# Optimization experiments

Measured on AMD Instinct MI355X. Metric: run time of the kernel, lower is better.

Reference implementation:

```python
import jax, jax.numpy as jnp
from jax import lax
import numpy as np

COST_CLASS, COST_BBOX, COST_GIOU = 2.0, 5.0, 2.0
ALPHA, GAMMA, OTA_K = 0.25, 2.0, 5
EXPANDED_STRIDES = 32.0
DEG = 180.0 / np.pi


def _make_corners(key, prefix):
    k1, k2, k3, k4, k5 = jax.random.split(key, 5)
    cx = jax.random.uniform(k1, prefix, minval=0.0, maxval=512.0)
    cy = jax.random.uniform(k2, prefix, minval=0.0, maxval=512.0)
    w = jax.random.uniform(k3, prefix, minval=8.0, maxval=128.0)
    h = jax.random.uniform(k4, prefix, minval=8.0, maxval=128.0)
    ang = jax.random.uniform(k5, prefix, minval=0.0, maxval=np.pi)
    offs = jnp.array([[-0.5, -0.5], [0.5, -0.5], [0.5, 0.5], [-0.5, 0.5]], jnp.float32)
    wh = jnp.stack([w, h], -1)[..., None, :]          # [..., 1, 2]
    pts = offs * wh                                    # [..., 4, 2]
    c, s = jnp.cos(ang)[..., None], jnp.sin(ang)[..., None]
    rx = pts[..., 0] * c - pts[..., 1] * s + cx[..., None]
    ry = pts[..., 0] * s + pts[..., 1] * c + cy[..., None]
    return jnp.stack([rx, ry], -1).reshape(prefix + (8,))


def setup_inputs() -> dict:
    key = jax.random.key(0)
    k1, k2, k3, k4 = jax.random.split(key, 4)
    B, Q, G, C = 16, 4096, 128, 80
    return {
        "pred_logits": jax.random.normal(k1, (B, Q, C), jnp.float32),
        "pred_boxes": _make_corners(k2, (B, Q)),
        "gt_boxes": _make_corners(k3, (B, G)),
        "gt_labels": jax.random.randint(k4, (B, G), 0, C),
    }


def corners_to_cxcywha(c):  # [N,8] -> [N,5]
    xc = (c[:, 0] + c[:, 2] + c[:, 4] + c[:, 6]) / 4
    yc = (c[:, 1] + c[:, 3] + c[:, 5] + c[:, 7]) / 4
    w = jnp.sqrt((c[:, 0] - c[:, 2]) ** 2 + (c[:, 1] - c[:, 3]) ** 2)
    h = jnp.sqrt((c[:, 2] - c[:, 4]) ** 2 + (c[:, 3] - c[:, 5]) ** 2)
    ang = jnp.arctan2(c[:, 3] - c[:, 1], c[:, 2] - c[:, 0]) * DEG
    return jnp.stack([xc, yc, w, h, ang], 1)


def _aabb(b5):
    cx, cy, w, h = b5[:, 0], b5[:, 1], b5[:, 2], b5[:, 3]
    return jnp.stack([cx - w / 2, cy - h / 2, cx + w / 2, cy + h / 2], 1)


def pairwise_iou(b1, b2):
    a, b = _aabb(b1), _aabb(b2)
    lt = jnp.maximum(a[:, None, :2], b[None, :, :2])
    rb = jnp.minimum(a[:, None, 2:], b[None, :, 2:])
    wh = jnp.clip(rb - lt, 0.0)
    inter = wh[..., 0] * wh[..., 1]
    area1 = (a[:, 2] - a[:, 0]) * (a[:, 3] - a[:, 1])
    area2 = (b[:, 2] - b[:, 0]) * (b[:, 3] - b[:, 1])
    return inter / (area1[:, None] + area2[None, :] - inter + 1e-8)


def pairwise_diou(b1, b2):
    iou = pairwise_iou(b1, b2)
    a, b = _aabb(b1), _aabb(b2)
    enc = jnp.maximum(a[:, None, 2:], b[None, :, 2:]) - jnp.minimum(a[:, None, :2], b[None, :, :2])
    c2 = (enc ** 2).sum(-1) + 1e-8
    d2 = ((b1[:, None, :2] - b2[None, :, :2]) ** 2).sum(-1)
    return iou - d2 / c2


def get_in_boxes_info(boxes, gts):
    bc = boxes.reshape(-1, 4, 2).mean(1)   # [Q,2]
    gp = gts.reshape(-1, 4, 2)             # [G,4,2]
    gc = gp.mean(1)                        # [G,2]
    cdist = jnp.sqrt(((bc[:, None] - gc[None]) ** 2).sum(-1))  # [Q,G]
    v1 = gp[:, 1] - gp[:, 0]
    v2 = gp[:, 2] - gp[:, 0]
    gt_area = jnp.abs(v1[:, 0] * v2[:, 1] - v1[:, 1] * v2[:, 0]) / 2
    diag = jnp.sqrt(((gp.max(1) - gp.min(1)) ** 2).sum(-1))
    radius = diag / EXPANDED_STRIDES
    in_boxes = cdist <= (gt_area / radius)[None, :]
    in_centers = cdist <= radius[None, :]
    return in_boxes.any(1), in_boxes & in_centers


def _dedup(cost, m):
    multi = m.sum(1) > 1
    onehot = jax.nn.one_hot(jnp.argmin(cost, 1), cost.shape[1], dtype=m.dtype)
    return jnp.where(multi[:, None], onehot, m)


def _match_single(logits, pboxes, gboxes, glabels):
    Q, G = pboxes.shape[0], gboxes.shape[0]
    prob = jax.nn.sigmoid(logits)
    fg_mask, _ = get_in_boxes_info(pboxes, gboxes)
    p5, g5 = corners_to_cxcywha(pboxes), corners_to_cxcywha(gboxes)
    ious = pairwise_iou(p5, g5)
    neg = (1 - ALPHA) * prob ** GAMMA * -jnp.log(1 - prob + 1e-8)
    pos = ALPHA * (1 - prob) ** GAMMA * -jnp.log(prob + 1e-8)
    cost_class = (pos - neg)[:, glabels]                         # [Q,G]
    cost_bbox = jnp.abs(pboxes[:, None] - gboxes[None]).sum(-1)  # L1 cdist on corners
    cost_giou = -pairwise_diou(p5, g5)
    # NB: source has `+ self.cost_giou * -cost_giou`, i.e. +w*diou; replicated verbatim.
    cost = COST_BBOX * cost_bbox + COST_CLASS * cost_class + COST_GIOU * (-cost_giou)
    cost = cost + 10000.0 * (~fg_mask)[:, None].astype(cost.dtype)
    # dynamic-k: sum of top OTA_K ious per gt, truncated to int, min 1
    topk = lax.top_k(ious.T, OTA_K)[0]                 # [G, k]
    dyn_k = jnp.clip(topk.sum(-1).astype(jnp.int32), 1, Q)
    ranks = jnp.argsort(jnp.argsort(cost, axis=0), axis=0)  # ascending-cost rank per column
    matching = (ranks < dyn_k[None, :]).astype(cost.dtype)
    matching = _dedup(cost, matching)
    # ensure every gt matched (bounded replication of the while loop)
    def cond(carry):
        c, m, it = carry
        return jnp.any(m.sum(0) == 0) & (it < G)
    def body(carry):
        c, m, it = carry
        c = c + 100000.0 * (m.sum(1) > 0)[:, None].astype(c.dtype)
        unm = m.sum(0) == 0
        amin = jnp.argmin(c, 0)                          # [G]
        hit = (jnp.arange(Q)[:, None] == amin[None, :]) & unm[None, :]
        m = jnp.where(hit, 1.0, m)
        m = _dedup(c, m)
        return (c, m, it + 1)
    _, matching, _ = lax.while_loop(cond, body, (cost, matching, jnp.int32(0)))
    return matching, cost, ious


def reference(pred_logits, pred_boxes, gt_boxes, gt_labels):
    return jax.vmap(_match_single)(pred_logits, pred_boxes, gt_boxes, gt_labels)
```

## Files before the change

kernel.cpp:

```cpp
#include <hip/hip_runtime.h>
#include <cstdint>
#include <cstddef>

#define B_ 16
#define Q_ 4096
#define G_ 128
#define C_ 80
#define QCHUNK 32
#define NCH (Q_ / QCHUNK)

typedef unsigned long long u64;
#define U64MAX 0xffffffffffffffffull

__device__ __forceinline__ u64 packkey(float v, int q) {
    unsigned int bts = __float_as_uint(v);
    if (bts == 0x80000000u) bts = 0u;
    bts = (bts & 0x80000000u) ? ~bts : (bts | 0x80000000u);
    return ((u64)bts << 32) | (unsigned int)q;
}

__device__ __forceinline__ u64 umin64(u64 a, u64 b) { return a < b ? a : b; }
__device__ __forceinline__ u64 umax64(u64 a, u64 b) { return a > b ? a : b; }

__device__ __forceinline__ void merge5_desc(
    float& a0, float& a1, float& a2, float& a3, float& a4,
    float b0, float b1, float b2, float b3, float b4)
{
    const float r0 = fmaxf(a0, b0);
    const float r1 = fmaxf(fmaxf(a1, b1), fminf(a0, b0));
    const float r2 = fmaxf(fmaxf(a2, b2), fmaxf(fminf(a0, b1), fminf(a1, b0)));
    const float r3 = fmaxf(fmaxf(a3, b3),
                     fmaxf(fminf(a0, b2), fmaxf(fminf(a1, b1), fminf(a2, b0))));
    const float r4 = fmaxf(fmaxf(a4, b4),
                     fmaxf(fmaxf(fminf(a0, b3), fminf(a3, b0)),
                           fmaxf(fminf(a1, b2), fminf(a2, b1))));
    a0 = r0; a1 = r1; a2 = r2; a3 = r3; a4 = r4;
}

__device__ __forceinline__ void merge5_asc(
    u64& a0, u64& a1, u64& a2, u64& a3, u64& a4,
    u64 b0, u64 b1, u64 b2, u64 b3, u64 b4)
{
    const u64 r0 = umin64(a0, b0);
    const u64 r1 = umin64(umin64(a1, b1), umax64(a0, b0));
    const u64 r2 = umin64(umin64(a2, b2), umin64(umax64(a0, b1), umax64(a1, b0)));
    const u64 r3 = umin64(umin64(a3, b3),
                   umin64(umax64(a0, b2), umin64(umax64(a1, b1), umax64(a2, b0))));
    const u64 r4 = umin64(umin64(a4, b4),
                   umin64(umin64(umax64(a0, b3), umax64(a3, b0)),
                          umin64(umax64(a1, b2), umax64(a2, b1))));
    a0 = r0; a1 = r1; a2 = r2; a3 = r3; a4 = r4;
}

__global__ __launch_bounds__(256) void posneg_kernel(
    const float* __restrict__ logits, float* __restrict__ posneg)
{
    const int i = blockIdx.x * 256 + threadIdx.x;
    const float x = logits[i];
    float p;
    if (x >= 0.f) { const float e = expf(-x); p = 1.f / (1.f + e); }
    else          { const float e = expf(x);  p = e / (1.f + e); }
    const float pos = 0.25f * (1.f - p) * (1.f - p) * (-logf(p + 1e-8f));
    const float neg = 0.75f * p * p * (-logf(1.f - p + 1e-8f));
    posneg[i] = pos - neg;
}

__global__ __launch_bounds__(256) void fused_cost_kernel(
    const float* __restrict__ posneg,
    const float* __restrict__ pboxes,
    const float* __restrict__ gboxes,
    const int*   __restrict__ glabels,
    float* __restrict__ out_cost,
    float* __restrict__ out_iou,
    float* __restrict__ costT,
    float* __restrict__ piou)
{
    const int tid = threadIdx.x;
    const int g   = tid & 127;
    const int qh  = tid >> 7;
    const int ci  = blockIdx.x, b = blockIdx.y;
    const int q0  = ci * QCHUNK;

    __shared__ float pq[QCHUNK][16];
    __shared__ int   fgf[QCHUNK];
    __shared__ float lbuf[16 * 80];
    __shared__ float ctile[QCHUNK][G_ + 1];
    __shared__ float phalf[G_][5];

    const float4* gb4 = (const float4*)(gboxes + ((size_t)b * G_ + g) * 8);
    const float4 gA = gb4[0], gB = gb4[1];
    const float g0 = gA.x, g1 = gA.y, g2 = gA.z, g3 = gA.w;
    const float g4 = gB.x, g5 = gB.y, g6 = gB.z, g7 = gB.w;
    const float gxc = (g0 + g2 + g4 + g6) * 0.25f;
    const float gyc = (g1 + g3 + g5 + g7) * 0.25f;
    const float gw = sqrtf((g0 - g2) * (g0 - g2) + (g1 - g3) * (g1 - g3));
    const float gh = sqrtf((g2 - g4) * (g2 - g4) + (g3 - g5) * (g3 - g5));
    const float gax0 = gxc - gw * 0.5f, gay0 = gyc - gh * 0.5f;
    const float gax1 = gxc + gw * 0.5f, gay1 = gyc + gh * 0.5f;
    const float garea = (gax1 - gax0) * (gay1 - gay0);
    const float v1x = g2 - g0, v1y = g3 - g1, v2x = g4 - g0, v2y = g5 - g1;
    const float gt_area = fabsf(v1x * v2y - v1y * v2x) * 0.5f;
    const float mxx = fmaxf(fmaxf(g0, g2), fmaxf(g4, g6));
    const float mnx = fminf(fminf(g0, g2), fminf(g4, g6));
    const float mxy = fmaxf(fmaxf(g1, g3), fmaxf(g5, g7));
    const float mny = fminf(fminf(g1, g3), fminf(g5, g7));
    const float dgx = mxx - mnx, dgy = mxy - mny;
    const float radius = sqrtf(dgx * dgx + dgy * dgy) / 32.0f;
    const float thresh = gt_area / radius;
    const int lab = glabels[b * G_ + g];

    if (tid < 64) {
        const float4 v = ((const float4*)(pboxes + ((size_t)b * Q_ + q0) * 8))[tid];
        *(float4*)&pq[tid >> 1][(tid & 1) * 4] = v;
    }
    __syncthreads();
    if (tid < QCHUNK) {
        const float* pr = pq[tid];
        const float p0 = pr[0], p1 = pr[1], p2 = pr[2], p3 = pr[3];
        const float p4 = pr[4], p5v = pr[5], p6 = pr[6], p7 = pr[7];
        const float pxc = (p0 + p2 + p4 + p6) * 0.25f;
        const float pyc = (p1 + p3 + p5v + p7) * 0.25f;
        const float pw = sqrtf((p0 - p2) * (p0 - p2) + (p1 - p3) * (p1 - p3));
        const float ph = sqrtf((p2 - p4) * (p2 - p4) + (p3 - p5v) * (p3 - p5v));
        pq[tid][8]  = pxc;
        pq[tid][9]  = pyc;
        pq[tid][10] = pxc - pw * 0.5f;
        pq[tid][11] = pyc - ph * 0.5f;
        pq[tid][12] = pxc + pw * 0.5f;
        pq[tid][13] = pyc + ph * 0.5f;
        pq[tid][14] = pw * ph;
        fgf[tid] = 0;
    }
    __syncthreads();

    const int lane0 = ((tid & 63) == 0);
    for (int i = 0; i < QCHUNK / 2; ++i) {
        const int ql = 2 * i + qh;
        const float dx = pq[ql][8] - gxc, dy = pq[ql][9] - gyc;
        const int in = sqrtf(dx * dx + dy * dy) <= thresh;
        const int anyin = __any(in);
        if (anyin && lane0) fgf[ql] = 1;
    }

    float t0 = -1e38f, t1 = -1e38f, t2 = -1e38f, t3 = -1e38f, t4 = -1e38f;

    for (int sc = 0; sc < QCHUNK / 16; ++sc) {
        __syncthreads();
        for (int j = tid; j < 16 * 80; j += 256)
            lbuf[j] = posneg[((size_t)b * Q_ + q0 + sc * 16) * 80 + j];
        __syncthreads();
        #pragma unroll
        for (int jj = 0; jj < 8; ++jj) {
            const int ql = sc * 16 + 2 * jj + qh;
            const int q  = q0 + ql;
            const float4 prA = *(const float4*)&pq[ql][0];
            const float4 prB = *(const float4*)&pq[ql][4];
            const float4 prC = *(const float4*)&pq[ql][8];
            const float4 prD = *(const float4*)&pq[ql][12];
            const float p0 = prA.x, p1 = prA.y, p2 = prA.z, p3 = prA.w;
            const float p4 = prB.x, p5v = prB.y, p6 = prB.z, p7 = prB.w;
            const float pxc = prC.x, pyc = prC.y;
            const float pax0 = prC.z, pay0 = prC.w, pax1 = prD.x, pay1 = prD.y;
            const float parea = prD.z;

            const float l1 = fabsf(p0 - g0) + fabsf(p1 - g1) + fabsf(p2 - g2)
                           + fabsf(p3 - g3) + fabsf(p4 - g4) + fabsf(p5v - g5)
                           + fabsf(p6 - g6) + fabsf(p7 - g7);

            const float ltx = fmaxf(pax0, gax0), lty = fmaxf(pay0, gay0);
            const float rbx = fminf(pax1, gax1), rby = fminf(pay1, gay1);
            const float iw = fmaxf(rbx - ltx, 0.f), ih = fmaxf(rby - lty, 0.f);
            const float inter = iw * ih;
            const float iou = inter / (parea + garea - inter + 1e-8f);

            const float ew = fmaxf(pax1, gax1) - fminf(pax0, gax0);
            const float eh = fmaxf(pay1, gay1) - fminf(pay0, gay0);
            const float cc2 = ew * ew + eh * eh + 1e-8f;
            const float dx = pxc - gxc, dy = pyc - gyc;
            const float diou = iou - (dx * dx + dy * dy) / cc2;

            const float cclass = lbuf[(2 * jj + qh) * 80 + lab];
            const float cost = 5.f * l1 + 2.f * cclass + 2.f * diou
                             + (fgf[ql] ? 0.f : 10000.f);

            const size_t o = ((size_t)b * Q_ + q) * G_ + g;
            out_cost[o] = cost;
            out_iou[o]  = iou;
            ctile[ql][g] = cost;

            if (iou > t4) {
                if (iou > t0)      { t4 = t3; t3 = t2; t2 = t1; t1 = t0; t0 = iou; }
                else if (iou > t1) { t4 = t3; t3 = t2; t2 = t1; t1 = iou; }
                else if (iou > t2) { t4 = t3; t3 = t2; t2 = iou; }
                else if (iou > t3) { t4 = t3; t3 = iou; }
                else               { t4 = iou; }
            }
        }
    }

    if (qh == 1) {
        phalf[g][0] = t0; phalf[g][1] = t1; phalf[g][2] = t2;
        phalf[g][3] = t3; phalf[g][4] = t4;
    }
    __syncthreads();
    if (qh == 0) {
        merge5_desc(t0, t1, t2, t3, t4,
                    phalf[g][0], phalf[g][1], phalf[g][2], phalf[g][3], phalf[g][4]);
        const size_t pbase = (((size_t)b * G_ + g) * NCH + ci) * 5;
        piou[pbase + 0] = t0; piou[pbase + 1] = t1; piou[pbase + 2] = t2;
        piou[pbase + 3] = t3; piou[pbase + 4] = t4;
    }

    for (int t = tid; t < QCHUNK * G_ / 4; t += 256) {
        const int gg = t >> 3;
        const int k  = (t & 7) << 2;
        float4 o;
        o.x = ctile[k + 0][gg]; o.y = ctile[k + 1][gg];
        o.z = ctile[k + 2][gg]; o.w = ctile[k + 3][gg];
        *(float4*)&costT[((size_t)b * G_ + gg) * Q_ + q0 + k] = o;
    }
}

__global__ __launch_bounds__(256) void ramin_kernel(
    const float* __restrict__ cost, int* __restrict__ ramin)
{
    const int wv = threadIdx.x >> 6, ln = threadIdx.x & 63;
    const int row = blockIdx.x * 4 + wv;
    const float2 c2v = ((const float2*)(cost + (size_t)row * G_))[ln];
    float v; int gg;
    if (c2v.x <= c2v.y) { v = c2v.x; gg = 2 * ln; }
    else                { v = c2v.y; gg = 2 * ln + 1; }
    for (int off = 32; off > 0; off >>= 1) {
        const float ov = __shfl_xor(v, off);
        const int   og = __shfl_xor(gg, off);
        if (ov < v || (ov == v && og < gg)) { v = ov; gg = og; }
    }
    if (ln == 0) ramin[row] = gg;
}

__global__ __launch_bounds__(256) void dynk_scatter_kernel(
    const float* __restrict__ costT,
    const float* __restrict__ piou,
    u64* __restrict__ cand,
    int* __restrict__ cnt,
    int* __restrict__ gsel)
{
    const int col = blockIdx.x;
    const int b = col >> 7, g = col & 127;
    const int tid = threadIdx.x;
    const int wv = tid >> 6, ln = tid & 63;

    __shared__ u64 wl[4][5];

    const float4* colp = (const float4*)(costT + (size_t)col * Q_);
    u64 k0 = U64MAX, k1 = U64MAX, k2 = U64MAX, k3 = U64MAX, k4 = U64MAX;
    #pragma unroll
    for (int s = 0; s < 4; ++s) {
        const int idx = tid + s * 256;
        const float4 c4 = colp[idx];
        const int qb = idx * 4;
        const float vv[4] = {c4.x, c4.y, c4.z, c4.w};
        #pragma unroll
        for (int j = 0; j < 4; ++j) {
            const u64 kk = packkey(vv[j], qb + j);
            if (kk < k4) {
                if (kk < k0)      { k4 = k3; k3 = k2; k2 = k1; k1 = k0; k0 = kk; }
                else if (kk < k1) { k4 = k3; k3 = k2; k2 = k1; k1 = kk; }
                else if (kk < k2) { k4 = k3; k3 = k2; k2 = kk; }
                else if (kk < k3) { k4 = k3; k3 = kk; }
                else              { k4 = kk; }
            }
        }
    }
    #pragma unroll
    for (int off = 1; off < 64; off <<= 1) {
        merge5_asc(k0, k1, k2, k3, k4,
                   __shfl_xor(k0, off), __shfl_xor(k1, off), __shfl_xor(k2, off),
                   __shfl_xor(k3, off), __shfl_xor(k4, off));
    }
    if (ln == 0) { wl[wv][0] = k0; wl[wv][1] = k1; wl[wv][2] = k2; wl[wv][3] = k3; wl[wv][4] = k4; }
    __syncthreads();

    float t0 = -1e38f, t1 = -1e38f, t2 = -1e38f, t3 = -1e38f, t4 = -1e38f;
    if (tid < 64) {
        const size_t base = (size_t)col * (NCH * 5) + (size_t)tid * 10;
        t0 = piou[base + 0]; t1 = piou[base + 1]; t2 = piou[base + 2];
        t3 = piou[base + 3]; t4 = piou[base + 4];
        merge5_desc(t0, t1, t2, t3, t4,
                    piou[base + 5], piou[base + 6], piou[base + 7],
                    piou[base + 8], piou[base + 9]);
        #pragma unroll
        for (int off = 1; off < 64; off <<= 1) {
            merge5_desc(t0, t1, t2, t3, t4,
                        __shfl_xor(t0, off), __shfl_xor(t1, off), __shfl_xor(t2, off),
                        __shfl_xor(t3, off), __shfl_xor(t4, off));
        }
    }

    if (tid == 0) {
        u64 f0 = wl[0][0], f1 = wl[0][1], f2 = wl[0][2], f3 = wl[0][3], f4 = wl[0][4];
        merge5_asc(f0, f1, f2, f3, f4, wl[1][0], wl[1][1], wl[1][2], wl[1][3], wl[1][4]);
        merge5_asc(f0, f1, f2, f3, f4, wl[2][0], wl[2][1], wl[2][2], wl[2][3], wl[2][4]);
        merge5_asc(f0, f1, f2, f3, f4, wl[3][0], wl[3][1], wl[3][2], wl[3][3], wl[3][4]);
        cand[(size_t)col * 5 + 0] = f0;
        cand[(size_t)col * 5 + 1] = f1;
        cand[(size_t)col * 5 + 2] = f2;
        cand[(size_t)col * 5 + 3] = f3;
        cand[(size_t)col * 5 + 4] = f4;

        const float s = t0 + t1 + t2 + t3 + t4;
        int dynk = (int)s;
        if (dynk < 1) dynk = 1;
        if (dynk > 5) dynk = 5;
        const u64 ks[5] = {f0, f1, f2, f3, f4};
        #pragma unroll
        for (int i = 0; i < 5; ++i) {
            if (i < dynk) {
                const int q = (int)(ks[i] & 0xffffffffu);
                atomicAdd(&cnt[b * Q_ + q], 1);
                gsel[b * Q_ + q] = g;
            }
        }
    }
}

__global__ __launch_bounds__(256) void loop_kernel(
    const float* __restrict__ costT,
    const int* __restrict__ cnt,
    const int* __restrict__ gsel,
    const int* __restrict__ ramin,
    const u64* __restrict__ cand,
    int* __restrict__ rmatch_final)
{
    const int b = blockIdx.x, tid = threadIdx.x;
    const int wv = tid >> 6, ln = tid & 63;

    __shared__ short rmatch[Q_];
    __shared__ unsigned char s_ra[Q_];
    __shared__ int newh[Q_];
    __shared__ unsigned char newg[Q_];
    __shared__ u64 scand[G_][5];
    __shared__ int ptrs[G_], col_cnt[G_], unm_list[G_], prop[G_], fb_slot[G_], touched[G_];
    __shared__ int n_unm, n_fb, n_touch;

    for (int q = tid; q < Q_; q += 256) {
        const int c  = cnt[b * Q_ + q];
        const int ra = ramin[b * Q_ + q];
        s_ra[q] = (unsigned char)ra;
        newh[q] = 0;
        rmatch[q] = (c == 0) ? (short)-1
                             : (c == 1 ? (short)gsel[b * Q_ + q] : (short)ra);
    }
    if (tid < G_) { col_cnt[tid] = 0; ptrs[tid] = 0; }
    for (int i = tid; i < G_ * 5; i += 256)
        scand[i / 5][i % 5] = cand[(size_t)b * G_ * 5 + i];
    __syncthreads();
    for (int q = tid; q < Q_; q += 256)
        if (rmatch[q] >= 0) atomicAdd(&col_cnt[rmatch[q]], 1);
    __syncthreads();

    for (int it = 0; it < G_; ++it) {
        if (tid == 0) { n_unm = 0; n_fb = 0; n_touch = 0; }
        __syncthreads();
        if (tid < G_ && col_cnt[tid] == 0)
            unm_list[atomicAdd(&n_unm, 1)] = tid;
        __syncthreads();
        const int nu = n_unm;
        if (nu == 0) break;

        if (tid < nu) {
            const int g = unm_list[tid];
            int p = ptrs[g];
            int q = -1;
            while (p < 5) {
                const int cq = (int)(scand[g][p] & 0xffffffffu);
                if (rmatch[cq] < 0) { q = cq; break; }
                ++p;
            }
            ptrs[g] = p;
            prop[tid] = q;
            if (q < 0) fb_slot[atomicAdd(&n_fb, 1)] = tid;
        }
        __syncthreads();

        const int nf = n_fb;
        for (int i = wv; i < nf; i += 4) {
            const int slot = fb_slot[i];
            const int g = unm_list[slot];
            const float4* colp = (const float4*)(costT + ((size_t)b * G_ + g) * Q_);
            u64 k0 = U64MAX, k1 = U64MAX, k2 = U64MAX, k3 = U64MAX, k4 = U64MAX;
            #pragma unroll 4
            for (int s = 0; s < Q_ / 256; ++s) {
                const int idx = ln + s * 64;
                const float4 c4 = colp[idx];
                const int qb = idx * 4;
                const float vv[4] = {c4.x, c4.y, c4.z, c4.w};
                #pragma unroll
                for (int j = 0; j < 4; ++j) {
                    if (rmatch[qb + j] < 0) {
                        const u64 kk = packkey(vv[j], qb + j);
                        if (kk < k4) {
                            if (kk < k0)      { k4 = k3; k3 = k2; k2 = k1; k1 = k0; k0 = kk; }
                            else if (kk < k1) { k4 = k3; k3 = k2; k2 = k1; k1 = kk; }
                            else if (kk < k2) { k4 = k3; k3 = k2; k2 = kk; }
                            else if (kk < k3) { k4 = k3; k3 = kk; }
                            else              { k4 = kk; }
                        }
                    }
                }
            }
            #pragma unroll
            for (int off = 1; off < 64; off <<= 1) {
                merge5_asc(k0, k1, k2, k3, k4,
                           __shfl_xor(k0, off), __shfl_xor(k1, off), __shfl_xor(k2, off),
                           __shfl_xor(k3, off), __shfl_xor(k4, off));
            }
            if (ln == 0) {
                scand[g][0] = k0; scand[g][1] = k1; scand[g][2] = k2;
                scand[g][3] = k3; scand[g][4] = k4;
                ptrs[g] = 0;
                prop[slot] = (int)(k0 & 0xffffffffu);
            }
        }
        __syncthreads();

        if (tid < nu) {
            const int q = prop[tid];
            newg[q] = (unsigned char)unm_list[tid];
            if (atomicAdd(&newh[q], 1) == 0)
                touched[atomicAdd(&n_touch, 1)] = q;
        }
        __syncthreads();

        const int nt = n_touch;
        if (tid < nt) {
            const int q = touched[tid];
            const int nh = newh[q];
            const int gg = (nh == 1) ? (int)newg[q] : (int)s_ra[q];
            rmatch[q] = (short)gg;
            atomicAdd(&col_cnt[gg], 1);
            newh[q] = 0;
        }
        __syncthreads();
    }

    for (int q = tid; q < Q_; q += 256)
        rmatch_final[b * Q_ + q] = rmatch[q];
}

__global__ __launch_bounds__(256) void expand_kernel(
    const int* __restrict__ rmatch_final, float* __restrict__ out_match)
{
    const int idx = blockIdx.x * 256 + threadIdx.x;
    const int row = idx >> 5;
    const int gb  = (idx & 31) << 2;
    const int rm  = rmatch_final[row];
    float4 o;
    o.x = (rm == gb)     ? 1.f : 0.f;
    o.y = (rm == gb + 1) ? 1.f : 0.f;
    o.z = (rm == gb + 2) ? 1.f : 0.f;
    o.w = (rm == gb + 3) ? 1.f : 0.f;
    ((float4*)out_match)[idx] = o;
}

extern "C" void kernel_launch(void* const* d_in, const int* in_sizes, int n_in,
                              void* d_out, int out_size, void* d_ws, size_t ws_size,
                              hipStream_t stream) {
    const float* logits  = (const float*)d_in[0];
    const float* pboxes  = (const float*)d_in[1];
    const float* gboxes  = (const float*)d_in[2];
    const int*   glabels = (const int*)d_in[3];

    float* out = (float*)d_out;
    const size_t BQG = (size_t)B_ * Q_ * G_;
    float* out_match = out;
    float* out_cost  = out + BQG;
    float* out_iou   = out + 2 * BQG;

    char* ws = (char*)d_ws;
    size_t off = 0;
    float* costT  = (float*)(ws + off); off += (size_t)B_ * G_ * Q_ * 4;
    float* posneg = (float*)(ws + off); off += (size_t)B_ * Q_ * C_ * 4;
    float* piou   = (float*)(ws + off); off += (size_t)B_ * G_ * NCH * 5 * 4;
    u64*   cand   = (u64*)  (ws + off); off += (size_t)B_ * G_ * 5 * 8;
    int*   ramin  = (int*)  (ws + off); off += (size_t)B_ * Q_ * 4;
    int*   cnt    = (int*)  (ws + off); off += (size_t)B_ * Q_ * 4;
    int*   gsel   = (int*)  (ws + off); off += (size_t)B_ * Q_ * 4;
    int*   rmf    = (int*)  (ws + off); off += (size_t)B_ * Q_ * 4;

    hipMemsetAsync(cnt, 0, (size_t)B_ * Q_ * 4, stream);
    posneg_kernel<<<B_ * Q_ * C_ / 256, 256, 0, stream>>>(logits, posneg);
    fused_cost_kernel<<<dim3(NCH, B_), 256, 0, stream>>>(
        posneg, pboxes, gboxes, glabels, out_cost, out_iou, costT, piou);
    ramin_kernel<<<B_ * Q_ / 4, 256, 0, stream>>>(out_cost, ramin);
    dynk_scatter_kernel<<<B_ * G_, 256, 0, stream>>>(costT, piou, cand, cnt, gsel);
    loop_kernel<<<B_, 256, 0, stream>>>(costT, cnt, gsel, ramin, cand, rmf);
    expand_kernel<<<(int)(BQG / 4 / 256), 256, 0, stream>>>(rmf, out_match);
}
```

Before: 214.9 us.

## Fuse focal-cost and row-argmin into the fused cost kernel

Result: no change. 211.4 us (-1.6%).

```diff
diff --git a/kernel.cpp b/kernel.cpp
--- a/kernel.cpp
+++ b/kernel.cpp
@@ -11,6 +11,10 @@
 
 typedef unsigned long long u64;
 #define U64MAX 0xffffffffffffffffull
+
+__device__ __forceinline__ bool lexless(float v1, int q1, float v2, int q2) {
+    return v1 < v2 || (v1 == v2 && q1 < q2);
+}
 
 __device__ __forceinline__ u64 packkey(float v, int q) {
     unsigned int bts = __float_as_uint(v);
@@ -52,28 +56,25 @@
     a0 = r0; a1 = r1; a2 = r2; a3 = r3; a4 = r4;
 }
 
-__global__ __launch_bounds__(256) void posneg_kernel(
-    const float* __restrict__ logits, float* __restrict__ posneg)
-{
-    const int i = blockIdx.x * 256 + threadIdx.x;
-    const float x = logits[i];
+__device__ __forceinline__ float focal_cost(float x) {
     float p;
     if (x >= 0.f) { const float e = expf(-x); p = 1.f / (1.f + e); }
     else          { const float e = expf(x);  p = e / (1.f + e); }
     const float pos = 0.25f * (1.f - p) * (1.f - p) * (-logf(p + 1e-8f));
     const float neg = 0.75f * p * p * (-logf(1.f - p + 1e-8f));
-    posneg[i] = pos - neg;
+    return pos - neg;
 }
 
 __global__ __launch_bounds__(256) void fused_cost_kernel(
-    const float* __restrict__ posneg,
+    const float* __restrict__ logits,
     const float* __restrict__ pboxes,
     const float* __restrict__ gboxes,
     const int*   __restrict__ glabels,
     float* __restrict__ out_cost,
     float* __restrict__ out_iou,
     float* __restrict__ costT,
-    float* __restrict__ piou)
+    float* __restrict__ piou,
+    int*   __restrict__ ramin)
 {
     const int tid = threadIdx.x;
     const int g   = tid & 127;
@@ -84,7 +85,7 @@
     __shared__ float pq[QCHUNK][16];
     __shared__ int   fgf[QCHUNK];
     __shared__ float lbuf[16 * 80];
-    __shared__ float ctile[QCHUNK][G_ + 1];
+    __shared__ float ctile[16][G_ + 1];
     __shared__ float phalf[G_][5];
 
     const float4* gb4 = (const float4*)(gboxes + ((size_t)b * G_ + g) * 8);
@@ -147,12 +148,13 @@
     for (int sc = 0; sc < QCHUNK / 16; ++sc) {
         __syncthreads();
         for (int j = tid; j < 16 * 80; j += 256)
-            lbuf[j] = posneg[((size_t)b * Q_ + q0 + sc * 16) * 80 + j];
+            lbuf[j] = focal_cost(logits[((size_t)b * Q_ + q0 + sc * 16) * 80 + j]);
         __syncthreads();
         #pragma unroll
         for (int jj = 0; jj < 8; ++jj) {
-            const int ql = sc * 16 + 2 * jj + qh;
-            const int q  = q0 + ql;
+            const int qls = 2 * jj + qh;
+            const int ql  = sc * 16 + qls;
+            const int q   = q0 + ql;
             const float4 prA = *(const float4*)&pq[ql][0];
             const float4 prB = *(const float4*)&pq[ql][4];
             const float4 prC = *(const float4*)&pq[ql][8];
@@ -179,14 +181,14 @@
             const float dx = pxc - gxc, dy = pyc - gyc;
             const float diou = iou - (dx * dx + dy * dy) / cc2;
 
-            const float cclass = lbuf[(2 * jj + qh) * 80 + lab];
+            const float cclass = lbuf[qls * 80 + lab];
             const float cost = 5.f * l1 + 2.f * cclass + 2.f * diou
                              + (fgf[ql] ? 0.f : 10000.f);
 
             const size_t o = ((size_t)b * Q_ + q) * G_ + g;
             out_cost[o] = cost;
             out_iou[o]  = iou;
-            ctile[ql][g] = cost;
+            ctile[qls][g] = cost;
 
             if (iou > t4) {
                 if (iou > t0)      { t4 = t3; t3 = t2; t2 = t1; t1 = t0; t0 = iou; }
@@ -195,6 +197,35 @@
                 else if (iou > t3) { t4 = t3; t3 = iou; }
                 else               { t4 = iou; }
             }
+        }
+        __syncthreads();
+
+        for (int t = tid; t < 16 * G_ / 4; t += 256) {
+            const int gg = t >> 2;
+            const int k  = (t & 3) << 2;
+            float4 o;
+            o.x = ctile[k + 0][gg]; o.y = ctile[k + 1][gg];
+            o.z = ctile[k + 2][gg]; o.w = ctile[k + 3][gg];
+            *(float4*)&costT[((size_t)b * G_ + gg) * Q_ + q0 + sc * 16 + k] = o;
+        }
+
+        {
+            const int qls  = tid >> 4;
+            const int part = tid & 15;
+            float v = 1e38f; int mg = 0x7fffffff;
+            #pragma unroll
+            for (int j = 0; j < 8; ++j) {
+                const int gg = part + 16 * j;
+                const float c = ctile[qls][gg];
+                if (c < v || (c == v && gg < mg)) { v = c; mg = gg; }
+            }
+            #pragma unroll
+            for (int off = 1; off < 16; off <<= 1) {
+                const float ov = __shfl_xor(v, off);
+                const int   og = __shfl_xor(mg, off);
+                if (ov < v || (ov == v && og < mg)) { v = ov; mg = og; }
+            }
+            if (part == 0) ramin[b * Q_ + q0 + sc * 16 + qls] = mg;
         }
     }
 
@@ -210,32 +241,6 @@
         piou[pbase + 0] = t0; piou[pbase + 1] = t1; piou[pbase + 2] = t2;
         piou[pbase + 3] = t3; piou[pbase + 4] = t4;
     }
-
-    for (int t = tid; t < QCHUNK * G_ / 4; t += 256) {
-        const int gg = t >> 3;
-        const int k  = (t & 7) << 2;
-        float4 o;
-        o.x = ctile[k + 0][gg]; o.y = ctile[k + 1][gg];
-        o.z = ctile[k + 2][gg]; o.w = ctile[k + 3][gg];
-        *(float4*)&costT[((size_t)b * G_ + gg) * Q_ + q0 + k] = o;
-    }
-}
-
-__global__ __launch_bounds__(256) void ramin_kernel(
-    const float* __restrict__ cost, int* __restrict__ ramin)
-{
-    const int wv = threadIdx.x >> 6, ln = threadIdx.x & 63;
-    const int row = blockIdx.x * 4 + wv;
-    const float2 c2v = ((const float2*)(cost + (size_t)row * G_))[ln];
-    float v; int gg;
-    if (c2v.x <= c2v.y) { v = c2v.x; gg = 2 * ln; }
-    else                { v = c2v.y; gg = 2 * ln + 1; }
-    for (int off = 32; off > 0; off >>= 1) {
-        const float ov = __shfl_xor(v, off);
-        const int   og = __shfl_xor(gg, off);
-        if (ov < v || (ov == v && og < gg)) { v = ov; gg = og; }
-    }
-    if (ln == 0) ramin[row] = gg;
 }
 
 __global__ __launch_bounds__(256) void dynk_scatter_kernel(
@@ -480,7 +485,6 @@
     char* ws = (char*)d_ws;
     size_t off = 0;
     float* costT  = (float*)(ws + off); off += (size_t)B_ * G_ * Q_ * 4;
-    float* posneg = (float*)(ws + off); off += (size_t)B_ * Q_ * C_ * 4;
     float* piou   = (float*)(ws + off); off += (size_t)B_ * G_ * NCH * 5 * 4;
     u64*   cand   = (u64*)  (ws + off); off += (size_t)B_ * G_ * 5 * 8;
     int*   ramin  = (int*)  (ws + off); off += (size_t)B_ * Q_ * 4;
@@ -489,10 +493,8 @@
     int*   rmf    = (int*)  (ws + off); off += (size_t)B_ * Q_ * 4;
 
     hipMemsetAsync(cnt, 0, (size_t)B_ * Q_ * 4, stream);
-    posneg_kernel<<<B_ * Q_ * C_ / 256, 256, 0, stream>>>(logits, posneg);
     fused_cost_kernel<<<dim3(NCH, B_), 256, 0, stream>>>(
-        posneg, pboxes, gboxes, glabels, out_cost, out_iou, costT, piou);
-    ramin_kernel<<<B_ * Q_ / 4, 256, 0, stream>>>(out_cost, ramin);
+        logits, pboxes, gboxes, glabels, out_cost, out_iou, costT, piou, ramin);
     dynk_scatter_kernel<<<B_ * G_, 256, 0, stream>>>(costT, piou, cand, cnt, gsel);
     loop_kernel<<<B_, 256, 0, stream>>>(costT, cnt, gsel, ramin, cand, rmf);
     expand_kernel<<<(int)(BQG / 4 / 256), 256, 0, stream>>>(rmf, out_match);
```
